# Optimization experiments

Measured on AMD Instinct MI355X. Metric: run time of the kernel, lower is better.

Reference implementation:

```python
import jax, jax.numpy as jnp
import numpy as np

# Dims: L layers, batch B, seq S, model dim D, heads H, ffn FF
L, B, S, D, H = 8, 2, 1024, 1024, 16
FF = 4 * D
HD = D // H
EPS = 1e-5  # torch LayerNorm default


def setup_inputs() -> dict:
    key = jax.random.key(0)
    ks = jax.random.split(key, 6)
    g = lambda k, shape, s: jax.random.normal(k, shape, jnp.float32) * s
    return {
        "x": g(ks[0], (B, S, D), 1.0),
        # True = masked out (code passes ~attn_mask to F.sdpa): causal mask
        "attn_mask": jnp.triu(jnp.ones((S, S), bool), 1),
        "qkv_w": g(ks[1], (L, 3 * D, D), 0.02),
        "qkv_b": jnp.zeros((L, 3 * D), jnp.float32),
        "out_w": g(ks[2], (L, D, D), 0.02),
        "out_b": jnp.zeros((L, D), jnp.float32),
        "w1": g(ks[3], (L, FF, D), 0.02),
        "b1": jnp.zeros((L, FF), jnp.float32),
        "w2": g(ks[4], (L, D, FF), 0.02),
        "b2": jnp.zeros((L, D), jnp.float32),
        "ln1_w": jnp.ones((L, D), jnp.float32),
        "ln1_b": jnp.zeros((L, D), jnp.float32),
        "ln2_w": jnp.ones((L, D), jnp.float32),
        "ln2_b": jnp.zeros((L, D), jnp.float32),
    }


def _layer_norm(x, w, b):
    m = jnp.mean(x, axis=-1, keepdims=True)
    v = jnp.var(x, axis=-1, keepdims=True)
    return (x - m) * jax.lax.rsqrt(v + EPS) * w + b


def _block(x, mask, qw, qb, ow, ob, w1, b1, w2, b2, l1w, l1b, l2w, l2b):
    # fused QKV projection: [B,S,3D]
    qkv = jnp.einsum("bsd,ed->bse", x, qw) + qb
    q, k, v = jnp.split(qkv, 3, axis=-1)
    k_cache, v_cache = k, v  # caches are stored pre-head-split [B,S,D]
    to_heads = lambda t: t.reshape(B, S, H, HD).transpose(0, 2, 1, 3)
    qh, kh, vh = to_heads(q), to_heads(k), to_heads(v)
    scores = jnp.einsum("bhqd,bhkd->bhqk", qh, kh) / jnp.sqrt(jnp.float32(HD))
    scores = jnp.where(mask, -jnp.inf, scores)  # mask True = disallowed
    attn = jnp.einsum("bhqk,bhkd->bhqd", jax.nn.softmax(scores, axis=-1), vh)
    attn = attn.transpose(0, 2, 1, 3).reshape(B, S, D)
    attn = jnp.einsum("bsd,ed->bse", attn, ow) + ob
    # post-LN residual + ReLU MLP + post-LN (padding_mask=None branch)
    x = _layer_norm(x + attn, l1w, l1b)
    h = jnp.einsum("bsf,df->bsd", jax.nn.relu(jnp.einsum("bsd,fd->bsf", x, w1) + b1), w2) + b2
    x = _layer_norm(x + h, l2w, l2b)
    return x, k_cache, v_cache


def reference(x, attn_mask, qkv_w, qkv_b, out_w, out_b, w1, b1, w2, b2,
              ln1_w, ln1_b, ln2_w, ln2_b):
    def step(carry, p):
        xc = carry
        xo, kc, vc = _block(xc, attn_mask, *p)
        return xo, (kc, vc)

    params = (qkv_w, qkv_b, out_w, out_b, w1, b1, w2, b2,
              ln1_w, ln1_b, ln2_w, ln2_b)
    x_out, (k_cache, v_cache) = jax.lax.scan(step, x, params)
    return x_out, k_cache, v_cache
```

## Files before the change

### kernel.cpp

```cpp
#include <hip/hip_runtime.h>
#include <cstdint>
#include <cstddef>
#include <math.h>

#define LL  8
#define BB  2
#define SS  1024
#define DD  1024
#define HH  16
#define HD  64
#define FFD 4096
#define BSD (BB*SS*DD)

typedef __attribute__((ext_vector_type(4))) float f32x4;
typedef __attribute__((ext_vector_type(8))) short bf16x8;
typedef __attribute__((ext_vector_type(4))) short bf16x4;

__device__ __forceinline__ unsigned short f2bf(float f) {
    unsigned u = __float_as_uint(f);
    unsigned r = (u + 0x7fffu + ((u >> 16) & 1u)) >> 16;
    return (unsigned short)r;
}

#define GLD16(gsrc, ldst) \
    __builtin_amdgcn_global_load_lds((const __attribute__((address_space(1))) void*)(gsrc), \
                                     (__attribute__((address_space(3))) void*)(ldst), 16, 0, 0)

__global__ __launch_bounds__(256)
void cvt_bf16(const float* __restrict__ in, unsigned short* __restrict__ out)
{
    size_t i = (size_t)blockIdx.x * 256 + threadIdx.x;
    float4 v = *(const float4*)(in + i * 4);
    ushort4 o;
    o.x = f2bf(v.x); o.y = f2bf(v.y); o.z = f2bf(v.z); o.w = f2bf(v.w);
    *(ushort4*)(out + i * 4) = o;
}

__global__ __launch_bounds__(512)
void gemm_bf16(const unsigned short* __restrict__ A, const unsigned short* __restrict__ W,
               const float* __restrict__ bias,
               float* __restrict__ C, unsigned short* __restrict__ Cb,
               float* __restrict__ Ck, float* __restrict__ Cv,
               unsigned short* __restrict__ Kb16, unsigned short* __restrict__ Vb16,
               int M, int N, int klen, int mode)
{
    __shared__ unsigned short lds[2][2 * 128 * 64];

    const int tid  = threadIdx.x;
    const int m0   = blockIdx.y * 128;
    const int n0   = blockIdx.x * 128;
    const int kbase= blockIdx.z * klen;
    const int lane = tid & 63;
    const int w    = tid >> 6;
    const int wr   = w >> 2;
    const int wc   = w & 3;
    const int lr   = lane & 15;
    const int kq   = lane >> 4;

    const int K = (mode == 3) ? (klen * gridDim.z) : klen;
    const int T = klen >> 6;

    const int srow0 = tid >> 3;
    const int spc0  = tid & 7;
    const int slc0  = spc0 ^ (srow0 & 7);
    const int srow1 = (tid + 512) >> 3;
    const int spc1  = (tid + 512) & 7;
    const int slc1  = spc1 ^ (srow1 & 7);

    #define STAGE_TILE(ti, dst)                                                   \
        do {                                                                      \
            const int kc = kbase + (ti) * 64;                                     \
            GLD16(A + (size_t)(m0 + srow0) * K + kc + slc0 * 8, (dst) + tid * 8); \
            GLD16(A + (size_t)(m0 + srow1) * K + kc + slc1 * 8, (dst) + 4096 + tid * 8); \
            GLD16(W + (size_t)(n0 + srow0) * K + kc + slc0 * 8, (dst) + 8192 + tid * 8); \
            GLD16(W + (size_t)(n0 + srow1) * K + kc + slc1 * 8, (dst) + 12288 + tid * 8); \
        } while (0)

    f32x4 acc[4][2];
    #pragma unroll
    for (int i = 0; i < 4; ++i)
        #pragma unroll
        for (int j = 0; j < 2; ++j) {
            f32x4 z = {0.f, 0.f, 0.f, 0.f};
            acc[i][j] = z;
        }

    STAGE_TILE(0, lds[0]);
    STAGE_TILE(1, lds[1]);

    for (int t = 0; t < T; ++t) {
        unsigned short* cb = lds[t & 1];

        if (t == T - 1) {
            asm volatile("s_waitcnt vmcnt(0)\n\ts_barrier" ::: "memory");
        } else {
            asm volatile("s_waitcnt vmcnt(4)\n\ts_barrier" ::: "memory");
        }

        bf16x8 a[4][2], b[2][2];
        #pragma unroll
        for (int mf = 0; mf < 4; ++mf) {
            const int r = wr * 64 + mf * 16 + lr;
            #pragma unroll
            for (int kk = 0; kk < 2; ++kk) {
                const int pc = (kk * 4 + kq) ^ (r & 7);
                a[mf][kk] = *(const bf16x8*)(cb + r * 64 + pc * 8);
            }
        }
        #pragma unroll
        for (int nf = 0; nf < 2; ++nf) {
            const int r = wc * 32 + nf * 16 + lr;
            #pragma unroll
            for (int kk = 0; kk < 2; ++kk) {
                const int pc = (kk * 4 + kq) ^ (r & 7);
                b[nf][kk] = *(const bf16x8*)(cb + 8192 + r * 64 + pc * 8);
            }
        }

        asm volatile("s_waitcnt lgkmcnt(0)\n\ts_barrier" ::: "memory");

        if (t + 2 < T) STAGE_TILE(t + 2, cb);
        __builtin_amdgcn_sched_barrier(0);

        __builtin_amdgcn_s_setprio(1);
        #pragma unroll
        for (int kk = 0; kk < 2; ++kk)
            #pragma unroll
            for (int mf = 0; mf < 4; ++mf)
                #pragma unroll
                for (int nf = 0; nf < 2; ++nf)
                    acc[mf][nf] = __builtin_amdgcn_mfma_f32_16x16x32_bf16(
                        a[mf][kk], b[nf][kk], acc[mf][nf], 0, 0, 0);
        __builtin_amdgcn_s_setprio(0);
    }
    #undef STAGE_TILE

    const int seg = n0 >> 10;
    float* Cp = (mode == 3) ? (C + (size_t)blockIdx.z * M * N) : C;
    #pragma unroll
    for (int nf = 0; nf < 2; ++nf) {
        const int cl = wc * 32 + nf * 16 + lr;
        const float bv = (mode == 3) ? 0.f : bias[n0 + cl];
        #pragma unroll
        for (int mf = 0; mf < 4; ++mf) {
            #pragma unroll
            for (int r = 0; r < 4; ++r) {
                const int row = m0 + wr * 64 + mf * 16 + kq * 4 + r;
                const float val = acc[mf][nf][r] + bv;
                if (mode == 2) {
                    const int col = (n0 & 1023) + cl;
                    float* dstf = (seg == 1) ? Ck : ((seg == 2) ? Cv : nullptr);
                    unsigned short* dstb = (seg == 0) ? Cb : ((seg == 1) ? Kb16 : Vb16);
                    if (dstf) dstf[(size_t)row * DD + col] = val;
                    dstb[(size_t)row * DD + col] = f2bf(val);
                } else if (mode == 1) {
                    Cb[(size_t)row * N + n0 + cl] = f2bf(fmaxf(val, 0.f));
                } else {
                    Cp[(size_t)row * N + n0 + cl] = val;
                }
            }
        }
    }
}

__global__ __launch_bounds__(256)
void attn_mfma(const unsigned short* __restrict__ Qb, const unsigned short* __restrict__ Kb,
               const unsigned short* __restrict__ Vb, unsigned short* __restrict__ ctxb)
{
    const int qt = blockIdx.x;
    const int h  = blockIdx.y;
    const int b  = blockIdx.z;
    const int tid  = threadIdx.x;
    const int lane = tid & 63;
    const int w    = tid >> 6;
    const int lr   = lane & 15;
    const int hi   = lane >> 4;

    __shared__ unsigned short smem[(64 + 64 + 4 * 16) * 68];
    unsigned short* Ks = smem;
    unsigned short* Vt = smem + 64 * 68;
    unsigned short* Pl = smem + 128 * 68 + w * 16 * 68;

    bf16x8 qa[2];
    {
        const unsigned short* qp =
            Qb + ((size_t)(b * SS + qt * 64 + w * 16 + lr)) * DD + h * HD;
        qa[0] = *(const bf16x8*)(qp + hi * 8);
        qa[1] = *(const bf16x8*)(qp + 32 + hi * 8);
    }

    f32x4 accO[4];
    #pragma unroll
    for (int t = 0; t < 4; ++t) { f32x4 z = {0.f,0.f,0.f,0.f}; accO[t] = z; }
    float m_run[4], l_run[4];
    #pragma unroll
    for (int r = 0; r < 4; ++r) { m_run[r] = -INFINITY; l_run[r] = 0.f; }

    for (int c = 0; c <= qt; ++c) {
        __syncthreads();
        const unsigned short* kb = Kb + ((size_t)(b * SS + c * 64)) * DD + h * HD;
        const unsigned short* vb = Vb + ((size_t)(b * SS + c * 64)) * DD + h * HD;
        #pragma unroll
        for (int i = 0; i < 2; ++i) {
            int e  = tid + i * 256;
            int r  = e >> 3, ch = e & 7;
            bf16x8 kv = *(const bf16x8*)(kb + (size_t)r * DD + ch * 8);
            *(bf16x4*)(Ks + r * 68 + ch * 8)     = __builtin_shufflevector(kv, kv, 0,1,2,3);
            *(bf16x4*)(Ks + r * 68 + ch * 8 + 4) = __builtin_shufflevector(kv, kv, 4,5,6,7);
            int k  = e & 63, d0 = (e >> 6) * 8;
            bf16x8 vv = *(const bf16x8*)(vb + (size_t)k * DD + d0);
            #pragma unroll
            for (int j = 0; j < 8; ++j)
                Vt[(d0 + j) * 68 + k] = (unsigned short)vv[j];
        }
        __syncthreads();

        f32x4 sa[4];
        #pragma unroll
        for (int t = 0; t < 4; ++t) { f32x4 z = {0.f,0.f,0.f,0.f}; sa[t] = z; }
        #pragma unroll
        for (int t = 0; t < 4; ++t) {
            #pragma unroll
            for (int s = 0; s < 2; ++s) {
                const unsigned short* bp = Ks + (t * 16 + lr) * 68 + s * 32 + hi * 8;
                bf16x4 b0 = *(const bf16x4*)bp;
                bf16x4 b1 = *(const bf16x4*)(bp + 4);
                bf16x8 bb = __builtin_shufflevector(b0, b1, 0,1,2,3,4,5,6,7);
                sa[t] = __builtin_amdgcn_mfma_f32_16x16x32_bf16(qa[s], bb, sa[t], 0, 0, 0);
            }
        }
        #pragma unroll
        for (int t = 0; t < 4; ++t)
            #pragma unroll
            for (int r = 0; r < 4; ++r)
                sa[t][r] *= 0.125f;
        if (c == qt) {
            const int qg = w * 16 + hi * 4;
            #pragma unroll
            for (int t = 0; t < 4; ++t)
                #pragma unroll
                for (int r = 0; r < 4; ++r)
                    if (t * 16 + lr > qg + r) sa[t][r] = -1e30f;
        }
        #pragma unroll
        for (int r = 0; r < 4; ++r) {
            float mx = fmaxf(fmaxf(sa[0][r], sa[1][r]), fmaxf(sa[2][r], sa[3][r]));
            mx = fmaxf(mx, __shfl_xor(mx, 1));
            mx = fmaxf(mx, __shfl_xor(mx, 2));
            mx = fmaxf(mx, __shfl_xor(mx, 4));
            mx = fmaxf(mx, __shfl_xor(mx, 8));
            const float mn = fmaxf(m_run[r], mx);
            float sum = 0.f;
            #pragma unroll
            for (int t = 0; t < 4; ++t) {
                float p = __expf(sa[t][r] - mn);
                sa[t][r] = p;
                sum += p;
            }
            sum += __shfl_xor(sum, 1);
            sum += __shfl_xor(sum, 2);
            sum += __shfl_xor(sum, 4);
            sum += __shfl_xor(sum, 8);
            const float sc = __expf(m_run[r] - mn);
            l_run[r] = l_run[r] * sc + sum;
            m_run[r] = mn;
            #pragma unroll
            for (int t = 0; t < 4; ++t) accO[t][r] *= sc;
        }
        #pragma unroll
        for (int t = 0; t < 4; ++t)
            #pragma unroll
            for (int r = 0; r < 4; ++r)
                Pl[(hi * 4 + r) * 68 + t * 16 + lr] = f2bf(sa[t][r]);

        #pragma unroll
        for (int s = 0; s < 2; ++s) {
            const unsigned short* ap = Pl + lr * 68 + s * 32 + hi * 8;
            bf16x4 a0 = *(const bf16x4*)ap;
            bf16x4 a1 = *(const bf16x4*)(ap + 4);
            bf16x8 aa = __builtin_shufflevector(a0, a1, 0,1,2,3,4,5,6,7);
            #pragma unroll
            for (int t = 0; t < 4; ++t) {
                const unsigned short* bp = Vt + (t * 16 + lr) * 68 + s * 32 + hi * 8;
                bf16x4 b0 = *(const bf16x4*)bp;
                bf16x4 b1 = *(const bf16x4*)(bp + 4);
                bf16x8 bb = __builtin_shufflevector(b0, b1, 0,1,2,3,4,5,6,7);
                accO[t] = __builtin_amdgcn_mfma_f32_16x16x32_bf16(aa, bb, accO[t], 0, 0, 0);
            }
        }
    }

    float inv[4];
    #pragma unroll
    for (int r = 0; r < 4; ++r) inv[r] = 1.f / l_run[r];

    __syncthreads();
    float* Of = (float*)smem;
    #pragma unroll
    for (int t = 0; t < 4; ++t)
        #pragma unroll
        for (int r = 0; r < 4; ++r)
            Of[(w * 16 + hi * 4 + r) * 68 + t * 16 + lr] = accO[t][r] * inv[r];
    __syncthreads();
    #pragma unroll
    for (int i = 0; i < 2; ++i) {
        int e = tid + i * 256;
        int r = e >> 3, ch = e & 7;
        const float* src = Of + r * 68 + ch * 8;
        float4 v0 = *(const float4*)(src);
        float4 v1 = *(const float4*)(src + 4);
        bf16x8 o;
        o[0] = (short)f2bf(v0.x); o[1] = (short)f2bf(v0.y);
        o[2] = (short)f2bf(v0.z); o[3] = (short)f2bf(v0.w);
        o[4] = (short)f2bf(v1.x); o[5] = (short)f2bf(v1.y);
        o[6] = (short)f2bf(v1.z); o[7] = (short)f2bf(v1.w);
        *(bf16x8*)(ctxb + ((size_t)(b * SS + qt * 64 + r)) * DD + h * HD + ch * 8) = o;
    }
}

__global__ __launch_bounds__(256)
void ln_kernel(float* __restrict__ x, const float* __restrict__ P,
               const float* __restrict__ bias,
               const float* __restrict__ w, const float* __restrict__ b,
               unsigned short* __restrict__ xb)
{
    const size_t PS = (size_t)BB * SS * DD;
    const int row = blockIdx.x;
    const int t   = threadIdx.x;
    float* xr = x + (size_t)row * DD;
    unsigned short* xbr = xb + (size_t)row * DD;

    float z[4];
    float s = 0.f, ss = 0.f;
    #pragma unroll
    for (int i = 0; i < 4; ++i) {
        int d = t + i * 256;
        size_t idx = (size_t)row * DD + d;
        float v = xr[d] + bias[d] + P[idx] + P[idx + PS] + P[idx + 2 * PS] + P[idx + 3 * PS];
        z[i] = v;
        s  += v;
        ss += v * v;
    }
    #pragma unroll
    for (int off = 32; off; off >>= 1) {
        s  += __shfl_down(s, off);
        ss += __shfl_down(ss, off);
    }
    __shared__ float sbuf[4], ssbuf[4];
    const int wave = t >> 6, lane = t & 63;
    if (lane == 0) { sbuf[wave] = s; ssbuf[wave] = ss; }
    __syncthreads();
    if (t == 0) {
        float S = 0.f, SSum = 0.f;
        #pragma unroll
        for (int i = 0; i < 4; ++i) { S += sbuf[i]; SSum += ssbuf[i]; }
        float mean = S * (1.f / 1024.f);
        float var  = SSum * (1.f / 1024.f) - mean * mean;
        sbuf[0]  = mean;
        ssbuf[0] = rsqrtf(var + 1e-5f);
    }
    __syncthreads();
    const float mean = sbuf[0], rstd = ssbuf[0];
    #pragma unroll
    for (int i = 0; i < 4; ++i) {
        int d = t + i * 256;
        float v = (z[i] - mean) * rstd * w[d] + b[d];
        xr[d]  = v;
        xbr[d] = f2bf(v);
    }
}

extern "C" void kernel_launch(void* const* d_in, const int* in_sizes, int n_in,
                              void* d_out, int out_size, void* d_ws, size_t ws_size,
                              hipStream_t stream)
{
    const float* x_in  = (const float*)d_in[0];
    const float* qkv_w = (const float*)d_in[2];
    const float* qkv_b = (const float*)d_in[3];
    const float* out_w = (const float*)d_in[4];
    const float* out_b = (const float*)d_in[5];
    const float* w1    = (const float*)d_in[6];
    const float* b1    = (const float*)d_in[7];
    const float* w2    = (const float*)d_in[8];
    const float* b2    = (const float*)d_in[9];
    const float* ln1w  = (const float*)d_in[10];
    const float* ln1b  = (const float*)d_in[11];
    const float* ln2w  = (const float*)d_in[12];
    const float* ln2b  = (const float*)d_in[13];

    float* out_x = (float*)d_out;
    float* out_k = out_x + (size_t)BSD;
    float* out_v = out_k + (size_t)LL * BSD;

    const size_t MEG = 1024 * 1024;
    float* ws = (float*)d_ws;
    float*          xbuf = ws;
    float*          part = ws + 2 * MEG;
    unsigned short* xb16 = (unsigned short*)(ws + 10 * MEG);
    unsigned short* ctxb = (unsigned short*)(ws + 11 * MEG);
    unsigned short* hb16 = (unsigned short*)(ws + 12 * MEG);
    unsigned short* qb16 = hb16;
    unsigned short* kb16 = hb16 + 2 * MEG;
    unsigned short* vb16 = hb16 + 4 * MEG;
    unsigned short* wAll = (unsigned short*)(ws + 16 * MEG);

    unsigned short* qkvW = wAll;
    unsigned short* outW = wAll + 24 * MEG;
    unsigned short* w1W  = wAll + 32 * MEG;
    unsigned short* w2W  = wAll + 64 * MEG;

    cvt_bf16<<<24 * MEG / 1024, 256, 0, stream>>>(qkv_w, qkvW);
    cvt_bf16<<< 8 * MEG / 1024, 256, 0, stream>>>(out_w, outW);
    cvt_bf16<<<32 * MEG / 1024, 256, 0, stream>>>(w1,    w1W);
    cvt_bf16<<<32 * MEG / 1024, 256, 0, stream>>>(w2,    w2W);

    hipMemcpyAsync(xbuf, x_in, (size_t)BSD * sizeof(float),
                   hipMemcpyDeviceToDevice, stream);
    cvt_bf16<<<BSD / 1024, 256, 0, stream>>>(x_in, xb16);

    const int M = BB * SS;

    for (int l = 0; l < LL; ++l) {
        const float* qb  = qkv_b + (size_t)l * 3 * DD;
        const float* ob  = out_b + (size_t)l * DD;
        const float* b1l = b1    + (size_t)l * FFD;
        const float* b2l = b2    + (size_t)l * DD;
        const unsigned short* qwl = qkvW + (size_t)l * 3 * DD * DD;
        const unsigned short* owl = outW + (size_t)l * DD * DD;
        const unsigned short* w1l = w1W  + (size_t)l * FFD * DD;
        const unsigned short* w2l = w2W  + (size_t)l * DD * FFD;
        float* kc = out_k + (size_t)l * BSD;
        float* vc = out_v + (size_t)l * BSD;

        gemm_bf16<<<dim3(3 * DD / 128, M / 128, 1), 512, 0, stream>>>(
            xb16, qwl, qb, nullptr, qb16, kc, vc, kb16, vb16, M, 3 * DD, DD, 2);

        attn_mfma<<<dim3(SS / 64, HH, BB), 256, 0, stream>>>(qb16, kb16, vb16, ctxb);

        gemm_bf16<<<dim3(DD / 128, M / 128, 4), 512, 0, stream>>>(
            ctxb, owl, nullptr, part, nullptr, nullptr, nullptr, nullptr, nullptr,
            M, DD, DD / 4, 3);

        ln_kernel<<<M, 256, 0, stream>>>(xbuf, part, ob,
                                         ln1w + (size_t)l * DD, ln1b + (size_t)l * DD, xb16);

        gemm_bf16<<<dim3(FFD / 128, M / 128, 1), 512, 0, stream>>>(
            xb16, w1l, b1l, nullptr, hb16, nullptr, nullptr, nullptr, nullptr,
            M, FFD, DD, 1);

        gemm_bf16<<<dim3(DD / 128, M / 128, 4), 512, 0, stream>>>(
            hb16, w2l, nullptr, part, nullptr, nullptr, nullptr, nullptr, nullptr,
            M, DD, FFD / 4, 3);

        ln_kernel<<<M, 256, 0, stream>>>(xbuf, part, b2l,
                                         ln2w + (size_t)l * DD, ln2b + (size_t)l * DD, xb16);
    }

    hipMemcpyAsync(out_x, xbuf, (size_t)BSD * sizeof(float),
                   hipMemcpyDeviceToDevice, stream);
}
```

Before: 1.354 ms.

## Store split-K partials as bf16, enlarge attention tiles, vectorize layernorm

Split-K GEMM partial sums are now written as bf16 instead of fp32, and the layernorm kernel reads them with vectorized loads. This halves partial-sum traffic at some accuracy cost. The attention kernel now processes 128 query rows per block with 512 threads and applies the causal mask per element on every chunk. The GEMM inner loop splits its LDS fragment loads into two k-halves, and the initial x copy is fused with the bf16 conversion into one kernel.

```diff
diff --git a/kernel.cpp b/kernel.cpp
--- a/kernel.cpp
+++ b/kernel.cpp
@@ -21,6 +21,9 @@
     unsigned r = (u + 0x7fffu + ((u >> 16) & 1u)) >> 16;
     return (unsigned short)r;
 }
+__device__ __forceinline__ float bf2f(unsigned short u) {
+    return __uint_as_float((unsigned)u << 16);
+}
 
 #define GLD16(gsrc, ldst) \
     __builtin_amdgcn_global_load_lds((const __attribute__((address_space(1))) void*)(gsrc), \
@@ -34,6 +37,18 @@
     ushort4 o;
     o.x = f2bf(v.x); o.y = f2bf(v.y); o.z = f2bf(v.z); o.w = f2bf(v.w);
     *(ushort4*)(out + i * 4) = o;
+}
+
+__global__ __launch_bounds__(256)
+void cvt_x(const float* __restrict__ in, float* __restrict__ outf,
+           unsigned short* __restrict__ outb)
+{
+    size_t i = (size_t)blockIdx.x * 256 + threadIdx.x;
+    float4 v = *(const float4*)(in + i * 4);
+    *(float4*)(outf + i * 4) = v;
+    ushort4 o;
+    o.x = f2bf(v.x); o.y = f2bf(v.y); o.z = f2bf(v.z); o.w = f2bf(v.w);
+    *(ushort4*)(outb + i * 4) = o;
 }
 
 __global__ __launch_bounds__(512)
@@ -97,24 +112,31 @@
             asm volatile("s_waitcnt vmcnt(4)\n\ts_barrier" ::: "memory");
         }
 
-        bf16x8 a[4][2], b[2][2];
+        bf16x8 a[4], b[2];
         #pragma unroll
         for (int mf = 0; mf < 4; ++mf) {
             const int r = wr * 64 + mf * 16 + lr;
-            #pragma unroll
-            for (int kk = 0; kk < 2; ++kk) {
-                const int pc = (kk * 4 + kq) ^ (r & 7);
-                a[mf][kk] = *(const bf16x8*)(cb + r * 64 + pc * 8);
-            }
+            const int pc = kq ^ (r & 7);
+            a[mf] = *(const bf16x8*)(cb + r * 64 + pc * 8);
         }
         #pragma unroll
         for (int nf = 0; nf < 2; ++nf) {
             const int r = wc * 32 + nf * 16 + lr;
-            #pragma unroll
-            for (int kk = 0; kk < 2; ++kk) {
-                const int pc = (kk * 4 + kq) ^ (r & 7);
-                b[nf][kk] = *(const bf16x8*)(cb + 8192 + r * 64 + pc * 8);
-            }
+            const int pc = kq ^ (r & 7);
+            b[nf] = *(const bf16x8*)(cb + 8192 + r * 64 + pc * 8);
+        }
+        bf16x8 a2[4], b2[2];
+        #pragma unroll
+        for (int mf = 0; mf < 4; ++mf) {
+            const int r = wr * 64 + mf * 16 + lr;
+            const int pc = (4 + kq) ^ (r & 7);
+            a2[mf] = *(const bf16x8*)(cb + r * 64 + pc * 8);
+        }
+        #pragma unroll
+        for (int nf = 0; nf < 2; ++nf) {
+            const int r = wc * 32 + nf * 16 + lr;
+            const int pc = (4 + kq) ^ (r & 7);
+            b2[nf] = *(const bf16x8*)(cb + 8192 + r * 64 + pc * 8);
         }
 
         asm volatile("s_waitcnt lgkmcnt(0)\n\ts_barrier" ::: "memory");
@@ -124,19 +146,22 @@
 
         __builtin_amdgcn_s_setprio(1);
         #pragma unroll
-        for (int kk = 0; kk < 2; ++kk)
-            #pragma unroll
-            for (int mf = 0; mf < 4; ++mf)
-                #pragma unroll
-                for (int nf = 0; nf < 2; ++nf)
-                    acc[mf][nf] = __builtin_amdgcn_mfma_f32_16x16x32_bf16(
-                        a[mf][kk], b[nf][kk], acc[mf][nf], 0, 0, 0);
+        for (int mf = 0; mf < 4; ++mf)
+            #pragma unroll
+            for (int nf = 0; nf < 2; ++nf)
+                acc[mf][nf] = __builtin_amdgcn_mfma_f32_16x16x32_bf16(
+                    a[mf], b[nf], acc[mf][nf], 0, 0, 0);
+        #pragma unroll
+        for (int mf = 0; mf < 4; ++mf)
+            #pragma unroll
+            for (int nf = 0; nf < 2; ++nf)
+                acc[mf][nf] = __builtin_amdgcn_mfma_f32_16x16x32_bf16(
+                    a2[mf], b2[nf], acc[mf][nf], 0, 0, 0);
         __builtin_amdgcn_s_setprio(0);
     }
     #undef STAGE_TILE
 
     const int seg = n0 >> 10;
-    float* Cp = (mode == 3) ? (C + (size_t)blockIdx.z * M * N) : C;
     #pragma unroll
     for (int nf = 0; nf < 2; ++nf) {
         const int cl = wc * 32 + nf * 16 + lr;
@@ -156,14 +181,14 @@
                 } else if (mode == 1) {
                     Cb[(size_t)row * N + n0 + cl] = f2bf(fmaxf(val, 0.f));
                 } else {
-                    Cp[(size_t)row * N + n0 + cl] = val;
+                    Cb[(size_t)blockIdx.z * M * N + (size_t)row * N + n0 + cl] = f2bf(val);
                 }
             }
         }
     }
 }
 
-__global__ __launch_bounds__(256)
+__global__ __launch_bounds__(512)
 void attn_mfma(const unsigned short* __restrict__ Qb, const unsigned short* __restrict__ Kb,
                const unsigned short* __restrict__ Vb, unsigned short* __restrict__ ctxb)
 {
@@ -176,15 +201,16 @@
     const int lr   = lane & 15;
     const int hi   = lane >> 4;
 
-    __shared__ unsigned short smem[(64 + 64 + 4 * 16) * 68];
+    __shared__ unsigned short smem[(64 + 64 + 8 * 16) * 68];
     unsigned short* Ks = smem;
     unsigned short* Vt = smem + 64 * 68;
     unsigned short* Pl = smem + 128 * 68 + w * 16 * 68;
 
+    const int qg0 = qt * 128 + w * 16;
+
     bf16x8 qa[2];
     {
-        const unsigned short* qp =
-            Qb + ((size_t)(b * SS + qt * 64 + w * 16 + lr)) * DD + h * HD;
+        const unsigned short* qp = Qb + ((size_t)(b * SS + qg0 + lr)) * DD + h * HD;
         qa[0] = *(const bf16x8*)(qp + hi * 8);
         qa[1] = *(const bf16x8*)(qp + 32 + hi * 8);
     }
@@ -196,18 +222,17 @@
     #pragma unroll
     for (int r = 0; r < 4; ++r) { m_run[r] = -INFINITY; l_run[r] = 0.f; }
 
-    for (int c = 0; c <= qt; ++c) {
+    const int nch = 2 * qt + 2;
+    for (int c = 0; c < nch; ++c) {
         __syncthreads();
         const unsigned short* kb = Kb + ((size_t)(b * SS + c * 64)) * DD + h * HD;
         const unsigned short* vb = Vb + ((size_t)(b * SS + c * 64)) * DD + h * HD;
-        #pragma unroll
-        for (int i = 0; i < 2; ++i) {
-            int e  = tid + i * 256;
-            int r  = e >> 3, ch = e & 7;
+        {
+            int r  = tid >> 3, ch = tid & 7;
             bf16x8 kv = *(const bf16x8*)(kb + (size_t)r * DD + ch * 8);
             *(bf16x4*)(Ks + r * 68 + ch * 8)     = __builtin_shufflevector(kv, kv, 0,1,2,3);
             *(bf16x4*)(Ks + r * 68 + ch * 8 + 4) = __builtin_shufflevector(kv, kv, 4,5,6,7);
-            int k  = e & 63, d0 = (e >> 6) * 8;
+            int k  = tid & 63, d0 = (tid >> 6) * 8;
             bf16x8 vv = *(const bf16x8*)(vb + (size_t)k * DD + d0);
             #pragma unroll
             for (int j = 0; j < 8; ++j)
@@ -230,17 +255,13 @@
             }
         }
         #pragma unroll
-        for (int t = 0; t < 4; ++t)
-            #pragma unroll
-            for (int r = 0; r < 4; ++r)
-                sa[t][r] *= 0.125f;
-        if (c == qt) {
-            const int qg = w * 16 + hi * 4;
-            #pragma unroll
-            for (int t = 0; t < 4; ++t)
-                #pragma unroll
-                for (int r = 0; r < 4; ++r)
-                    if (t * 16 + lr > qg + r) sa[t][r] = -1e30f;
+        for (int t = 0; t < 4; ++t) {
+            #pragma unroll
+            for (int r = 0; r < 4; ++r) {
+                const int kg = c * 64 + t * 16 + lr;
+                const int qg = qg0 + hi * 4 + r;
+                sa[t][r] = (kg > qg) ? -1e30f : sa[t][r] * 0.125f;
+            }
         }
         #pragma unroll
         for (int r = 0; r < 4; ++r) {
@@ -304,7 +325,7 @@
     __syncthreads();
     #pragma unroll
     for (int i = 0; i < 2; ++i) {
-        int e = tid + i * 256;
+        int e = tid + i * 512;
         int r = e >> 3, ch = e & 7;
         const float* src = Of + r * 68 + ch * 8;
         float4 v0 = *(const float4*)(src);
@@ -314,33 +335,35 @@
         o[2] = (short)f2bf(v0.z); o[3] = (short)f2bf(v0.w);
         o[4] = (short)f2bf(v1.x); o[5] = (short)f2bf(v1.y);
         o[6] = (short)f2bf(v1.z); o[7] = (short)f2bf(v1.w);
-        *(bf16x8*)(ctxb + ((size_t)(b * SS + qt * 64 + r)) * DD + h * HD + ch * 8) = o;
+        *(bf16x8*)(ctxb + ((size_t)(b * SS + qt * 128 + r)) * DD + h * HD + ch * 8) = o;
     }
 }
 
 __global__ __launch_bounds__(256)
-void ln_kernel(float* __restrict__ x, const float* __restrict__ P,
+void ln_kernel(float* __restrict__ x, const unsigned short* __restrict__ P,
                const float* __restrict__ bias,
                const float* __restrict__ w, const float* __restrict__ b,
                unsigned short* __restrict__ xb)
 {
-    const size_t PS = (size_t)BB * SS * DD;
+    const size_t PS = (size_t)BSD;
     const int row = blockIdx.x;
     const int t   = threadIdx.x;
+    const int d0  = t * 4;
     float* xr = x + (size_t)row * DD;
     unsigned short* xbr = xb + (size_t)row * DD;
-
-    float z[4];
-    float s = 0.f, ss = 0.f;
-    #pragma unroll
-    for (int i = 0; i < 4; ++i) {
-        int d = t + i * 256;
-        size_t idx = (size_t)row * DD + d;
-        float v = xr[d] + bias[d] + P[idx] + P[idx + PS] + P[idx + 2 * PS] + P[idx + 3 * PS];
-        z[i] = v;
-        s  += v;
-        ss += v * v;
-    }
+    const size_t base = (size_t)row * DD + d0;
+
+    float4 xv = *(const float4*)(xr + d0);
+    float4 bv = *(const float4*)(bias + d0);
+    float z[4] = {xv.x + bv.x, xv.y + bv.y, xv.z + bv.z, xv.w + bv.w};
+    #pragma unroll
+    for (int p = 0; p < 4; ++p) {
+        ushort4 pv = *(const ushort4*)(P + base + p * PS);
+        z[0] += bf2f(pv.x); z[1] += bf2f(pv.y); z[2] += bf2f(pv.z); z[3] += bf2f(pv.w);
+    }
+    float s = z[0] + z[1] + z[2] + z[3];
+    float ss = z[0]*z[0] + z[1]*z[1] + z[2]*z[2] + z[3]*z[3];
+
     #pragma unroll
     for (int off = 32; off; off >>= 1) {
         s  += __shfl_down(s, off);
@@ -361,13 +384,17 @@
     }
     __syncthreads();
     const float mean = sbuf[0], rstd = ssbuf[0];
-    #pragma unroll
-    for (int i = 0; i < 4; ++i) {
-        int d = t + i * 256;
-        float v = (z[i] - mean) * rstd * w[d] + b[d];
-        xr[d]  = v;
-        xbr[d] = f2bf(v);
-    }
+
+    float4 wv = *(const float4*)(w + d0);
+    float4 bb = *(const float4*)(b + d0);
+    float o0 = (z[0] - mean) * rstd * wv.x + bb.x;
+    float o1 = (z[1] - mean) * rstd * wv.y + bb.y;
+    float o2 = (z[2] - mean) * rstd * wv.z + bb.z;
+    float o3 = (z[3] - mean) * rstd * wv.w + bb.w;
+    *(float4*)(xr + d0) = make_float4(o0, o1, o2, o3);
+    ushort4 ob4;
+    ob4.x = f2bf(o0); ob4.y = f2bf(o1); ob4.z = f2bf(o2); ob4.w = f2bf(o3);
+    *(ushort4*)(xbr + d0) = ob4;
 }
 
 extern "C" void kernel_launch(void* const* d_in, const int* in_sizes, int n_in,
@@ -394,15 +421,15 @@
 
     const size_t MEG = 1024 * 1024;
     float* ws = (float*)d_ws;
-    float*          xbuf = ws;
-    float*          part = ws + 2 * MEG;
-    unsigned short* xb16 = (unsigned short*)(ws + 10 * MEG);
-    unsigned short* ctxb = (unsigned short*)(ws + 11 * MEG);
-    unsigned short* hb16 = (unsigned short*)(ws + 12 * MEG);
-    unsigned short* qb16 = hb16;
-    unsigned short* kb16 = hb16 + 2 * MEG;
-    unsigned short* vb16 = hb16 + 4 * MEG;
-    unsigned short* wAll = (unsigned short*)(ws + 16 * MEG);
+    float*          xbuf  = ws;
+    unsigned short* part16= (unsigned short*)(ws + 2 * MEG);
+    unsigned short* xb16  = (unsigned short*)(ws + 6 * MEG);
+    unsigned short* ctxb  = (unsigned short*)(ws + 7 * MEG);
+    unsigned short* hb16  = (unsigned short*)(ws + 8 * MEG);
+    unsigned short* qb16  = hb16;
+    unsigned short* kb16  = hb16 + 2 * MEG;
+    unsigned short* vb16  = hb16 + 4 * MEG;
+    unsigned short* wAll  = (unsigned short*)(ws + 12 * MEG);
 
     unsigned short* qkvW = wAll;
     unsigned short* outW = wAll + 24 * MEG;
@@ -413,10 +440,7 @@
     cvt_bf16<<< 8 * MEG / 1024, 256, 0, stream>>>(out_w, outW);
     cvt_bf16<<<32 * MEG / 1024, 256, 0, stream>>>(w1,    w1W);
     cvt_bf16<<<32 * MEG / 1024, 256, 0, stream>>>(w2,    w2W);
-
-    hipMemcpyAsync(xbuf, x_in, (size_t)BSD * sizeof(float),
-                   hipMemcpyDeviceToDevice, stream);
-    cvt_bf16<<<BSD / 1024, 256, 0, stream>>>(x_in, xb16);
+    cvt_x<<<BSD / 1024, 256, 0, stream>>>(x_in, xbuf, xb16);
 
     const int M = BB * SS;
 
@@ -435,13 +459,13 @@
         gemm_bf16<<<dim3(3 * DD / 128, M / 128, 1), 512, 0, stream>>>(
             xb16, qwl, qb, nullptr, qb16, kc, vc, kb16, vb16, M, 3 * DD, DD, 2);
 
-        attn_mfma<<<dim3(SS / 64, HH, BB), 256, 0, stream>>>(qb16, kb16, vb16, ctxb);
+        attn_mfma<<<dim3(SS / 128, HH, BB), 512, 0, stream>>>(qb16, kb16, vb16, ctxb);
 
         gemm_bf16<<<dim3(DD / 128, M / 128, 4), 512, 0, stream>>>(
-            ctxb, owl, nullptr, part, nullptr, nullptr, nullptr, nullptr, nullptr,
+            ctxb, owl, nullptr, nullptr, part16, nullptr, nullptr, nullptr, nullptr,
             M, DD, DD / 4, 3);
 
-        ln_kernel<<<M, 256, 0, stream>>>(xbuf, part, ob,
+        ln_kernel<<<M, 256, 0, stream>>>(xbuf, part16, ob,
                                          ln1w + (size_t)l * DD, ln1b + (size_t)l * DD, xb16);
 
         gemm_bf16<<<dim3(FFD / 128, M / 128, 1), 512, 0, stream>>>(
@@ -449,10 +473,10 @@
             M, FFD, DD, 1);
 
         gemm_bf16<<<dim3(DD / 128, M / 128, 4), 512, 0, stream>>>(
-            hb16, w2l, nullptr, part, nullptr, nullptr, nullptr, nullptr, nullptr,
+            hb16, w2l, nullptr, nullptr, part16, nullptr, nullptr, nullptr, nullptr,
             M, DD, FFD / 4, 3);
 
-        ln_kernel<<<M, 256, 0, stream>>>(xbuf, part, b2l,
+        ln_kernel<<<M, 256, 0, stream>>>(xbuf, part16, b2l,
                                          ln2w + (size_t)l * DD, ln2b + (size_t)l * DD, xb16);
     }
 
```

Measured after the change: 1.284 ms. 5.2% less time.
